# Kernel optimization log

Measured on AMD Instinct MI355X. Metric: run time of the kernel, lower is better.

Reference implementation:

```python
import jax, jax.numpy as jnp
import numpy as np

EPS_LN = 1e-5
NEG_SLOPE = 0.2
NUM_GRAPHS = 64


def layer_norm(h, g, b):
    mu = h.mean(-1, keepdims=True)
    var = ((h - mu) ** 2).mean(-1, keepdims=True)
    return (h - mu) * jax.lax.rsqrt(var + EPS_LN) * g + b


def segment_softmax(alpha, dst, n):
    # alpha: [E2, H], softmax over edges sharing the same dst node
    m = jax.ops.segment_max(alpha, dst, num_segments=n)
    m = jnp.where(jnp.isfinite(m), m, 0.0)
    e = jnp.exp(alpha - m[dst])
    s = jax.ops.segment_sum(e, dst, num_segments=n)
    return e / (s[dst] + 1e-16)


def gat_conv(h, src, dst, eattr, W, We, a_s, a_d, a_e, bias, H, C):
    # PyG GATConv: shared src/dst linear, edge features, self-loops (fill='mean')
    N = h.shape[0]
    x = (h @ W).reshape(N, H, C)  # [N,H,C]
    loop = jnp.arange(N)
    src2 = jnp.concatenate([src, loop])
    dst2 = jnp.concatenate([dst, loop])
    loop_attr = jnp.broadcast_to(eattr.mean(0, keepdims=True), (N, eattr.shape[1]))
    e2 = jnp.concatenate([eattr, loop_attr], 0)
    eh = (e2 @ We).reshape(-1, H, C)  # [E2,H,C]
    alpha = (x * a_s).sum(-1)[src2] + (x * a_d).sum(-1)[dst2] + (eh * a_e).sum(-1)
    alpha = jax.nn.leaky_relu(alpha, NEG_SLOPE)  # [E2,H]
    alpha = segment_softmax(alpha, dst2, N)
    out = jax.ops.segment_sum(x[src2] * alpha[:, :, None], dst2, num_segments=N)
    return out.reshape(N, H * C) + bias


def setup_inputs():
    key = jax.random.key(0)
    ks = jax.random.split(key, 24)
    N, E = 50000, 400000
    Fin, Hd, H, ed = 6, 64, 4, 1
    d0 = Hd * H          # 256 after layer0
    C1 = 128 // H        # 32, layer1 per-head out
    s = 0.1
    inp = {
        'x': jax.random.normal(ks[0], (N, Fin), jnp.float32),
        'edge_index': jax.random.randint(ks[1], (2, E), 0, N),
        'edge_attr': jax.random.uniform(ks[2], (E, ed), jnp.float32),
        'batch': jnp.sort(jax.random.randint(ks[3], (N,), 0, NUM_GRAPHS)),
        'W_in': jax.random.normal(ks[4], (Fin, Hd), jnp.float32) * s,
        'b_in': jnp.zeros((Hd,), jnp.float32),
        'l0_W': jax.random.normal(ks[5], (Hd, H * Hd), jnp.float32) * s,
        'l0_We': jax.random.normal(ks[6], (ed, H * Hd), jnp.float32) * s,
        'l0_as': jax.random.normal(ks[7], (H, Hd), jnp.float32) * s,
        'l0_ad': jax.random.normal(ks[8], (H, Hd), jnp.float32) * s,
        'l0_ae': jax.random.normal(ks[9], (H, Hd), jnp.float32) * s,
        'l0_b': jnp.zeros((H * Hd,), jnp.float32),
        'ln0_g': jnp.ones((d0,), jnp.float32),
        'ln0_b': jnp.zeros((d0,), jnp.float32),
        'l1_W': jax.random.normal(ks[10], (d0, H * C1), jnp.float32) * s,
        'l1_We': jax.random.normal(ks[11], (ed, H * C1), jnp.float32) * s,
        'l1_as': jax.random.normal(ks[12], (H, C1), jnp.float32) * s,
        'l1_ad': jax.random.normal(ks[13], (H, C1), jnp.float32) * s,
        'l1_ae': jax.random.normal(ks[14], (H, C1), jnp.float32) * s,
        'l1_b': jnp.zeros((H * C1,), jnp.float32),
        'ln1_g': jnp.ones((128,), jnp.float32),
        'ln1_b': jnp.zeros((128,), jnp.float32),
    }
    return inp


def reference(x, edge_index, edge_attr, batch, W_in, b_in,
              l0_W, l0_We, l0_as, l0_ad, l0_ae, l0_b, ln0_g, ln0_b,
              l1_W, l1_We, l1_as, l1_ad, l1_ae, l1_b, ln1_g, ln1_b):
    src, dst = edge_index[0], edge_index[1]
    H = 4
    h = x @ W_in + b_in                                  # input_proj
    h = gat_conv(h, src, dst, edge_attr, l0_W, l0_We, l0_as, l0_ad, l0_ae, l0_b, H, 64)
    h = layer_norm(h, ln0_g, ln0_b)
    h = jax.nn.elu(h)                                    # dropout off (eval)
    h = gat_conv(h, src, dst, edge_attr, l1_W, l1_We, l1_as, l1_ad, l1_ae, l1_b, H, 32)
    h = layer_norm(h, ln1_g, ln1_b)
    cnt = jax.ops.segment_sum(jnp.ones((h.shape[0],), h.dtype), batch, num_segments=NUM_GRAPHS)
    h_mean = jax.ops.segment_sum(h, batch, num_segments=NUM_GRAPHS) / jnp.maximum(cnt, 1.0)[:, None]
    h_max = jax.ops.segment_max(h, batch, num_segments=NUM_GRAPHS)
    return (h_mean + h_max) / 2.0
```

## Files before the change

### kernel.cpp

```cpp
#include <hip/hip_runtime.h>
#include <math.h>

#define EPS_LN   1e-5f
#define NEG_SLOPE 0.2f
#define NUM_GRAPHS 64
#define POOL_SPLIT 16

__device__ __forceinline__ float red64(float v) {
    #pragma unroll
    for (int m = 32; m > 0; m >>= 1) v += __shfl_xor(v, m);
    return v;
}

__global__ __launch_bounds__(256) void k_input_proj(
    const float* __restrict__ x, const float* __restrict__ Win,
    const float* __restrict__ bin, float* __restrict__ h, int N)
{
    int t = blockIdx.x * 256 + threadIdx.x;
    if (t >= N * 64) return;
    int n = t >> 6, c = t & 63;
    float acc = bin[c];
    const float* xr = x + n * 6;
    #pragma unroll
    for (int k = 0; k < 6; ++k) acc += xr[k] * Win[k * 64 + c];
    h[t] = acc;
}

__global__ __launch_bounds__(256) void k_prep(
    const float* __restrict__ We0, const float* __restrict__ ae0,
    const float* __restrict__ We1, const float* __restrict__ ae1,
    float* __restrict__ wedot0, float* __restrict__ wedot1)
{
    __shared__ float red[256];
    int t = threadIdx.x;
    red[t] = We0[t] * ae0[t];
    __syncthreads();
    for (int s = 32; s > 0; s >>= 1) { if ((t & 63) < s) red[t] += red[t + s]; __syncthreads(); }
    if ((t & 63) == 0) wedot0[t >> 6] = red[t];
    __syncthreads();
    red[t] = (t < 128) ? We1[t] * ae1[t] : 0.f;
    __syncthreads();
    for (int s = 16; s > 0; s >>= 1) { if (t < 128 && (t & 31) < s) red[t] += red[t + s]; __syncthreads(); }
    if (t < 128 && (t & 31) == 0) wedot1[t >> 5] = red[t];
}

__global__ __launch_bounds__(256) void k_esum_partial(const float* __restrict__ ea, float* __restrict__ part, int E)
{
    __shared__ float red[256];
    int t = threadIdx.x;
    float s = 0.f;
    for (int i = blockIdx.x * 256 + t; i < E; i += gridDim.x * 256) s += ea[i];
    red[t] = s; __syncthreads();
    for (int k = 128; k > 0; k >>= 1) { if (t < k) red[t] += red[t + k]; __syncthreads(); }
    if (t == 0) part[blockIdx.x] = red[0];
}
__global__ __launch_bounds__(256) void k_esum_final(const float* __restrict__ part, int B, float* __restrict__ mean_out, int E)
{
    __shared__ float red[256];
    int t = threadIdx.x;
    red[t] = (t < B) ? part[t] : 0.f; __syncthreads();
    for (int k = 128; k > 0; k >>= 1) { if (t < k) red[t] += red[t + k]; __syncthreads(); }
    if (t == 0) *mean_out = red[0] / (float)E;
}

__global__ __launch_bounds__(256) void k_counts_init(int* __restrict__ counts, int N)
{
    int t = blockIdx.x * 256 + threadIdx.x;
    if (t < N) counts[t] = 1;
}
__global__ __launch_bounds__(256) void k_count(const int* __restrict__ dst, int* __restrict__ counts, int E)
{
    int e = blockIdx.x * 256 + threadIdx.x;
    if (e < E) atomicAdd(&counts[dst[e]], 1);
}
__global__ __launch_bounds__(256) void k_scan_partial(const int* __restrict__ counts, int* __restrict__ bsum, int N)
{
    __shared__ int red[256];
    int b = blockIdx.x, t = threadIdx.x;
    int base = b * 1024 + t * 4;
    int s = 0;
    #pragma unroll
    for (int i = 0; i < 4; ++i) { int idx = base + i; if (idx < N) s += counts[idx]; }
    red[t] = s; __syncthreads();
    for (int k = 128; k > 0; k >>= 1) { if (t < k) red[t] += red[t + k]; __syncthreads(); }
    if (t == 0) bsum[b] = red[0];
}
__global__ __launch_bounds__(64) void k_scan_bsums(const int* __restrict__ bsum, int* __restrict__ bpre, int B)
{
    __shared__ int s[64];
    int t = threadIdx.x;
    int v = (t < B) ? bsum[t] : 0;
    s[t] = v; __syncthreads();
    for (int off = 1; off < 64; off <<= 1) {
        int u = (t >= off) ? s[t - off] : 0; __syncthreads();
        s[t] += u; __syncthreads();
    }
    if (t < B) bpre[t] = s[t] - v;
}
__global__ __launch_bounds__(256) void k_scan_chunk(
    const int* __restrict__ counts, const int* __restrict__ bpre,
    int* __restrict__ row_ptr, int* __restrict__ cursor, int N, int E2)
{
    __shared__ int s[256];
    int b = blockIdx.x, t = threadIdx.x;
    int base = b * 1024 + t * 4;
    int l0 = (base + 0 < N) ? counts[base + 0] : 0;
    int l1 = (base + 1 < N) ? counts[base + 1] : 0;
    int l2 = (base + 2 < N) ? counts[base + 2] : 0;
    int l3 = (base + 3 < N) ? counts[base + 3] : 0;
    int lsum = l0 + l1 + l2 + l3;
    s[t] = lsum; __syncthreads();
    for (int off = 1; off < 256; off <<= 1) {
        int u = (t >= off) ? s[t - off] : 0; __syncthreads();
        s[t] += u; __syncthreads();
    }
    int run = bpre[b] + s[t] - lsum;
    if (base + 0 < N) { row_ptr[base + 0] = run; cursor[base + 0] = run; } run += l0;
    if (base + 1 < N) { row_ptr[base + 1] = run; cursor[base + 1] = run; } run += l1;
    if (base + 2 < N) { row_ptr[base + 2] = run; cursor[base + 2] = run; } run += l2;
    if (base + 3 < N) { row_ptr[base + 3] = run; cursor[base + 3] = run; }
    if (b == 0 && t == 0) row_ptr[N] = E2;
}
__global__ __launch_bounds__(256) void k_place(
    const int* __restrict__ dst, int* __restrict__ cursor, int* __restrict__ eids, int E, int N)
{
    int e = blockIdx.x * 256 + threadIdx.x;
    if (e >= E + N) return;
    int d = (e < E) ? dst[e] : (e - E);
    int pos = atomicAdd(&cursor[d], 1);
    eids[pos] = e;
}
__global__ __launch_bounds__(256) void k_rowsort(const int* __restrict__ row_ptr, int* __restrict__ eids, int N)
{
    int n = blockIdx.x * 256 + threadIdx.x;
    if (n >= N) return;
    int r0 = row_ptr[n], r1 = row_ptr[n + 1];
    for (int i = r0 + 1; i < r1; ++i) {
        int key = eids[i];
        int j = i - 1;
        while (j >= r0 && eids[j] > key) { eids[j + 1] = eids[j]; --j; }
        eids[j + 1] = key;
    }
}

__global__ __launch_bounds__(256) void k_gemm0(
    const float* __restrict__ h, const float* __restrict__ W0,
    const float* __restrict__ As, const float* __restrict__ Ad,
    float* __restrict__ x0, float* __restrict__ as0, float* __restrict__ ad0, int N)
{
    __shared__ float Wc[32 * 128];
    __shared__ float Ht[32 * 128];
    const int nb = blockIdx.x * 128;
    const int q  = blockIdx.y;
    const int t = threadIdx.x;
    const int tc = t & 15, tr = t >> 4;
    const int r0 = tr * 4, c0 = tc * 4;
    const int kg = t & 7, rb = t >> 3;
    float asv[8], adv[8];
    #pragma unroll
    for (int j = 0; j < 8; ++j) {
        int col = q * 128 + c0 + ((j < 4) ? j : 60 + j);
        asv[j] = As[col]; adv[j] = Ad[col];
    }
    float acc[8][8] = {};
    #pragma unroll
    for (int kc = 0; kc < 2; ++kc) {
        __syncthreads();
        #pragma unroll
        for (int j = 0; j < 4; ++j) {
            int row = rb + j * 32;
            int n = nb + row;
            float4 v = make_float4(0.f, 0.f, 0.f, 0.f);
            if (n < N)
                v = *reinterpret_cast<const float4*>(h + (size_t)n * 64 + kc * 32 + kg * 4);
            #pragma unroll
            for (int i = 0; i < 4; ++i) {
                int k = kg * 4 + i;
                float e = (i == 0) ? v.x : (i == 1) ? v.y : (i == 2) ? v.z : v.w;
                Ht[k * 128 + (row ^ (k & 28))] = e;
            }
        }
        #pragma unroll
        for (int it = 0; it < 4; ++it) {
            int idx = t * 4 + it * 1024;
            int k2 = idx >> 7, c = idx & 127;
            *reinterpret_cast<float4*>(&Wc[idx]) =
                *reinterpret_cast<const float4*>(W0 + (size_t)(kc * 32 + k2) * 256 + q * 128 + c);
        }
        __syncthreads();
        #pragma unroll 4
        for (int k2 = 0; k2 < 32; ++k2) {
            int sw = k2 & 28;
            float4 hlo = *reinterpret_cast<const float4*>(&Ht[k2 * 128 + (r0 ^ sw)]);
            float4 hhi = *reinterpret_cast<const float4*>(&Ht[k2 * 128 + ((r0 + 64) ^ sw)]);
            float4 wlo = *reinterpret_cast<const float4*>(&Wc[k2 * 128 + c0]);
            float4 whi = *reinterpret_cast<const float4*>(&Wc[k2 * 128 + c0 + 64]);
            float hr[8] = {hlo.x, hlo.y, hlo.z, hlo.w, hhi.x, hhi.y, hhi.z, hhi.w};
            float wr[8] = {wlo.x, wlo.y, wlo.z, wlo.w, whi.x, whi.y, whi.z, whi.w};
            #pragma unroll
            for (int i = 0; i < 8; ++i)
                #pragma unroll
                for (int j = 0; j < 8; ++j)
                    acc[i][j] += hr[i] * wr[j];
        }
    }
    #pragma unroll
    for (int i = 0; i < 8; ++i) {
        int n = nb + ((i < 4) ? (r0 + i) : (r0 + 60 + i));
        if (n < N) {
            *reinterpret_cast<float4*>(x0 + (size_t)n * 256 + q * 128 + c0) =
                make_float4(acc[i][0], acc[i][1], acc[i][2], acc[i][3]);
            *reinterpret_cast<float4*>(x0 + (size_t)n * 256 + q * 128 + c0 + 64) =
                make_float4(acc[i][4], acc[i][5], acc[i][6], acc[i][7]);
        }
        float sA = acc[i][0] * asv[0] + acc[i][1] * asv[1] + acc[i][2] * asv[2] + acc[i][3] * asv[3];
        float sB = acc[i][4] * asv[4] + acc[i][5] * asv[5] + acc[i][6] * asv[6] + acc[i][7] * asv[7];
        float dA = acc[i][0] * adv[0] + acc[i][1] * adv[1] + acc[i][2] * adv[2] + acc[i][3] * adv[3];
        float dB = acc[i][4] * adv[4] + acc[i][5] * adv[5] + acc[i][6] * adv[6] + acc[i][7] * adv[7];
        #pragma unroll
        for (int off = 1; off <= 8; off <<= 1) {
            sA += __shfl_xor(sA, off); sB += __shfl_xor(sB, off);
            dA += __shfl_xor(dA, off); dB += __shfl_xor(dB, off);
        }
        if (tc == 0 && n < N) {
            as0[n * 4 + 2 * q] = sA; as0[n * 4 + 2 * q + 1] = sB;
            ad0[n * 4 + 2 * q] = dA; ad0[n * 4 + 2 * q + 1] = dB;
        }
    }
}

__global__ __launch_bounds__(256) void k_gemm1(
    const float* __restrict__ h0, const float* __restrict__ W1,
    const float* __restrict__ As, const float* __restrict__ Ad,
    float* __restrict__ x1, float* __restrict__ as1, float* __restrict__ ad1, int N)
{
    __shared__ float Wc[32 * 128];
    __shared__ float Ht[32 * 128];
    const int nb = blockIdx.x * 128;
    const int t = threadIdx.x;
    const int tc = t & 15, tr = t >> 4;
    const int r0 = tr * 4, c0 = tc * 4;
    const int kg = t & 7, rb = t >> 3;
    float asv[8], adv[8];
    #pragma unroll
    for (int j = 0; j < 8; ++j) {
        int col = c0 + ((j < 4) ? j : 60 + j);
        asv[j] = As[col]; adv[j] = Ad[col];
    }
    float acc[8][8] = {};
    for (int kc = 0; kc < 8; ++kc) {
        __syncthreads();
        #pragma unroll
        for (int j = 0; j < 4; ++j) {
            int row = rb + j * 32;
            int n = nb + row;
            float4 v = make_float4(0.f, 0.f, 0.f, 0.f);
            if (n < N)
                v = *reinterpret_cast<const float4*>(h0 + (size_t)n * 256 + kc * 32 + kg * 4);
            #pragma unroll
            for (int i = 0; i < 4; ++i) {
                int k = kg * 4 + i;
                float e = (i == 0) ? v.x : (i == 1) ? v.y : (i == 2) ? v.z : v.w;
                Ht[k * 128 + (row ^ (k & 28))] = e;
            }
        }
        #pragma unroll
        for (int it = 0; it < 4; ++it) {
            int idx = t * 4 + it * 1024;
            int k2 = idx >> 7, c = idx & 127;
            *reinterpret_cast<float4*>(&Wc[idx]) =
                *reinterpret_cast<const float4*>(W1 + (size_t)(kc * 32 + k2) * 128 + c);
        }
        __syncthreads();
        #pragma unroll 4
        for (int k2 = 0; k2 < 32; ++k2) {
            int sw = k2 & 28;
            float4 hlo = *reinterpret_cast<const float4*>(&Ht[k2 * 128 + (r0 ^ sw)]);
            float4 hhi = *reinterpret_cast<const float4*>(&Ht[k2 * 128 + ((r0 + 64) ^ sw)]);
            float4 wlo = *reinterpret_cast<const float4*>(&Wc[k2 * 128 + c0]);
            float4 whi = *reinterpret_cast<const float4*>(&Wc[k2 * 128 + c0 + 64]);
            float hr[8] = {hlo.x, hlo.y, hlo.z, hlo.w, hhi.x, hhi.y, hhi.z, hhi.w};
            float wr[8] = {wlo.x, wlo.y, wlo.z, wlo.w, whi.x, whi.y, whi.z, whi.w};
            #pragma unroll
            for (int i = 0; i < 8; ++i)
                #pragma unroll
                for (int j = 0; j < 8; ++j)
                    acc[i][j] += hr[i] * wr[j];
        }
    }
    #pragma unroll
    for (int i = 0; i < 8; ++i) {
        int n = nb + ((i < 4) ? (r0 + i) : (r0 + 60 + i));
        if (n < N) {
            *reinterpret_cast<float4*>(x1 + (size_t)n * 128 + c0) =
                make_float4(acc[i][0], acc[i][1], acc[i][2], acc[i][3]);
            *reinterpret_cast<float4*>(x1 + (size_t)n * 128 + c0 + 64) =
                make_float4(acc[i][4], acc[i][5], acc[i][6], acc[i][7]);
        }
        float sA = acc[i][0] * asv[0] + acc[i][1] * asv[1] + acc[i][2] * asv[2] + acc[i][3] * asv[3];
        float sB = acc[i][4] * asv[4] + acc[i][5] * asv[5] + acc[i][6] * asv[6] + acc[i][7] * asv[7];
        float dA = acc[i][0] * adv[0] + acc[i][1] * adv[1] + acc[i][2] * adv[2] + acc[i][3] * adv[3];
        float dB = acc[i][4] * adv[4] + acc[i][5] * adv[5] + acc[i][6] * adv[6] + acc[i][7] * adv[7];
        #pragma unroll
        for (int off = 1; off <= 4; off <<= 1) {
            sA += __shfl_xor(sA, off); sB += __shfl_xor(sB, off);
            dA += __shfl_xor(dA, off); dB += __shfl_xor(dB, off);
        }
        if ((tc & 7) == 0 && n < N) {
            int hA = tc >> 3;
            as1[n * 4 + hA] = sA; as1[n * 4 + 2 + hA] = sB;
            ad1[n * 4 + hA] = dA; ad1[n * 4 + 2 + hA] = dB;
        }
    }
}

template <bool WRITE_SRC>
__global__ __launch_bounds__(256) void k_edgeprep(
    const int* __restrict__ row_ptr, const int* __restrict__ eids,
    const int* __restrict__ src, const float* __restrict__ eattr,
    const float* __restrict__ emean_p, const float* __restrict__ wedot,
    const float* __restrict__ as_n, const float* __restrict__ ad_n,
    int* __restrict__ srcp, float4* __restrict__ alpha, float* __restrict__ sinv,
    int N, int E)
{
    int n = (blockIdx.x * 256 + threadIdx.x) >> 6;
    int lane = threadIdx.x & 63;
    if (n >= N) return;
    float emean = *emean_p;
    float wd0 = wedot[0], wd1 = wedot[1], wd2 = wedot[2], wd3 = wedot[3];
    float adv0 = ad_n[n * 4 + 0], adv1 = ad_n[n * 4 + 1];
    float adv2 = ad_n[n * 4 + 2], adv3 = ad_n[n * 4 + 3];
    int r0 = row_ptr[n], r1 = row_ptr[n + 1];

    float m0 = -1e30f, m1 = -1e30f, m2 = -1e30f, m3 = -1e30f;
    for (int i = r0 + lane; i < r1; i += 64) {
        int eid = eids[i];
        int sn; float ev;
        if (eid < E) { sn = src[eid]; ev = eattr[eid]; } else { sn = n; ev = emean; }
        if (WRITE_SRC) srcp[i] = sn;
        const float* as4 = as_n + (size_t)sn * 4;
        float a0 = as4[0] + adv0 + ev * wd0;
        float a1 = as4[1] + adv1 + ev * wd1;
        float a2 = as4[2] + adv2 + ev * wd2;
        float a3 = as4[3] + adv3 + ev * wd3;
        a0 = (a0 > 0.f) ? a0 : NEG_SLOPE * a0;
        a1 = (a1 > 0.f) ? a1 : NEG_SLOPE * a1;
        a2 = (a2 > 0.f) ? a2 : NEG_SLOPE * a2;
        a3 = (a3 > 0.f) ? a3 : NEG_SLOPE * a3;
        m0 = fmaxf(m0, a0); m1 = fmaxf(m1, a1);
        m2 = fmaxf(m2, a2); m3 = fmaxf(m3, a3);
        alpha[i] = make_float4(a0, a1, a2, a3);
    }
    #pragma unroll
    for (int off = 32; off > 0; off >>= 1) {
        m0 = fmaxf(m0, __shfl_xor(m0, off));
        m1 = fmaxf(m1, __shfl_xor(m1, off));
        m2 = fmaxf(m2, __shfl_xor(m2, off));
        m3 = fmaxf(m3, __shfl_xor(m3, off));
    }
    float s0 = 0.f, s1 = 0.f, s2 = 0.f, s3 = 0.f;
    for (int i = r0 + lane; i < r1; i += 64) {
        float4 a = alpha[i];
        float w0 = __expf(a.x - m0), w1 = __expf(a.y - m1);
        float w2 = __expf(a.z - m2), w3 = __expf(a.w - m3);
        s0 += w0; s1 += w1; s2 += w2; s3 += w3;
        alpha[i] = make_float4(w0, w1, w2, w3);
    }
    #pragma unroll
    for (int off = 32; off > 0; off >>= 1) {
        s0 += __shfl_xor(s0, off); s1 += __shfl_xor(s1, off);
        s2 += __shfl_xor(s2, off); s3 += __shfl_xor(s3, off);
    }
    if (lane == 0) {
        sinv[n * 4 + 0] = 1.f / (s0 + 1e-16f);
        sinv[n * 4 + 1] = 1.f / (s1 + 1e-16f);
        sinv[n * 4 + 2] = 1.f / (s2 + 1e-16f);
        sinv[n * 4 + 3] = 1.f / (s3 + 1e-16f);
    }
}

template <int HC, int VEC, bool DO_ELU>
__global__ __launch_bounds__(256) void k_agg(
    const float* __restrict__ x, const int* __restrict__ row_ptr,
    const int* __restrict__ srcp, const float* __restrict__ alpha,
    const float* __restrict__ sinv,
    const float* __restrict__ bias, const float* __restrict__ lng, const float* __restrict__ lnb,
    float* __restrict__ out, int N)
{
    int n = (blockIdx.x * 256 + threadIdx.x) >> 6;
    int lane = threadIdx.x & 63;
    if (n >= N) return;
    int hh = lane >> 4;
    int r0 = row_ptr[n], r1 = row_ptr[n + 1];

    float acc[VEC] = {};
    for (int i = r0; i < r1; i += 8) {
        int cnt = min(r1 - i, 8);
        int sn[8]; float wv[8];
        #pragma unroll
        for (int j = 0; j < 8; ++j)
            if (j < cnt) { sn[j] = srcp[i + j]; wv[j] = alpha[(size_t)(i + j) * 4 + hh]; }
        #pragma unroll
        for (int j = 0; j < 8; ++j)
            if (j < cnt) {
                const float* xr = x + (size_t)sn[j] * HC + lane * VEC;
                if constexpr (VEC == 4) {
                    float4 xv = *reinterpret_cast<const float4*>(xr);
                    acc[0] += wv[j] * xv.x; acc[1] += wv[j] * xv.y;
                    acc[2] += wv[j] * xv.z; acc[3] += wv[j] * xv.w;
                } else {
                    float2 xv = *reinterpret_cast<const float2*>(xr);
                    acc[0] += wv[j] * xv.x; acc[1] += wv[j] * xv.y;
                }
            }
    }
    float inv = sinv[n * 4 + hh];

    int ch0 = lane * VEC;
    float v[VEC];
    #pragma unroll
    for (int i = 0; i < VEC; ++i) v[i] = acc[i] * inv + bias[ch0 + i];
    float ls = 0.f;
    #pragma unroll
    for (int i = 0; i < VEC; ++i) ls += v[i];
    ls = red64(ls);
    float mu = ls / (float)HC;
    float lv = 0.f;
    #pragma unroll
    for (int i = 0; i < VEC; ++i) { float d = v[i] - mu; lv += d * d; }
    lv = red64(lv);
    float rs = rsqrtf(lv / (float)HC + EPS_LN);
    float o[VEC];
    #pragma unroll
    for (int i = 0; i < VEC; ++i) {
        float y = (v[i] - mu) * rs * lng[ch0 + i] + lnb[ch0 + i];
        if (DO_ELU) y = (y > 0.f) ? y : (expm1f(y));
        o[i] = y;
    }
    float* orow = out + (size_t)n * HC + ch0;
    if constexpr (VEC == 4) *reinterpret_cast<float4*>(orow) = make_float4(o[0], o[1], o[2], o[3]);
    else                    *reinterpret_cast<float2*>(orow) = make_float2(o[0], o[1]);
}

__global__ __launch_bounds__(128) void k_bounds(const int* __restrict__ batch, int* __restrict__ gstart, int N)
{
    int g = threadIdx.x;
    if (g > NUM_GRAPHS) return;
    int lo = 0, hi = N;
    while (lo < hi) { int mid = (lo + hi) >> 1; if (batch[mid] < g) lo = mid + 1; else hi = mid; }
    gstart[g] = lo;
}
__global__ __launch_bounds__(128) void k_pool1(
    const float* __restrict__ h1, const int* __restrict__ gstart,
    float* __restrict__ psum, float* __restrict__ pmax)
{
    int g = blockIdx.x, sl = blockIdx.y, c = threadIdx.x;
    int s0 = gstart[g], s1 = gstart[g + 1];
    int cnt = s1 - s0;
    int chunk = (cnt + POOL_SPLIT - 1) / POOL_SPLIT;
    int b0 = s0 + sl * chunk;
    int b1 = min(b0 + chunk, s1);
    float sum = 0.f, mx = -INFINITY;
    for (int n = b0; n < b1; ++n) {
        float v = h1[(size_t)n * 128 + c];
        sum += v; mx = fmaxf(mx, v);
    }
    int o = (g * POOL_SPLIT + sl) * 128 + c;
    psum[o] = sum; pmax[o] = mx;
}
__global__ __launch_bounds__(128) void k_pool2(
    const float* __restrict__ psum, const float* __restrict__ pmax,
    const int* __restrict__ gstart, float* __restrict__ out)
{
    int g = blockIdx.x, c = threadIdx.x;
    float sum = 0.f, mx = -INFINITY;
    #pragma unroll
    for (int sl = 0; sl < POOL_SPLIT; ++sl) {
        int o = (g * POOL_SPLIT + sl) * 128 + c;
        sum += psum[o];
        mx = fmaxf(mx, pmax[o]);
    }
    int cnt = gstart[g + 1] - gstart[g];
    float mean = sum / fmaxf((float)cnt, 1.f);
    out[g * 128 + c] = 0.5f * (mean + mx);
}

extern "C" void kernel_launch(void* const* d_in, const int* in_sizes, int n_in,
                              void* d_out, int out_size, void* d_ws, size_t ws_size,
                              hipStream_t stream)
{
    const float* x     = (const float*)d_in[0];
    const int*   ei    = (const int*)d_in[1];
    const float* eattr = (const float*)d_in[2];
    const int*   batch = (const int*)d_in[3];
    const float* Win   = (const float*)d_in[4];
    const float* bin   = (const float*)d_in[5];
    const float* l0W   = (const float*)d_in[6];
    const float* l0We  = (const float*)d_in[7];
    const float* l0as  = (const float*)d_in[8];
    const float* l0ad  = (const float*)d_in[9];
    const float* l0ae  = (const float*)d_in[10];
    const float* l0b   = (const float*)d_in[11];
    const float* ln0g  = (const float*)d_in[12];
    const float* ln0b  = (const float*)d_in[13];
    const float* l1W   = (const float*)d_in[14];
    const float* l1We  = (const float*)d_in[15];
    const float* l1as  = (const float*)d_in[16];
    const float* l1ad  = (const float*)d_in[17];
    const float* l1ae  = (const float*)d_in[18];
    const float* l1b   = (const float*)d_in[19];
    const float* ln1g  = (const float*)d_in[20];
    const float* ln1b  = (const float*)d_in[21];

    const int N = in_sizes[0] / 6;
    const int E = in_sizes[1] / 2;
    const int E2 = E + N;
    const int* srcI = ei;
    const int* dstI = ei + E;

    char* ws = (char*)d_ws;
    size_t off = 0;
    auto alloc = [&](size_t bytes) -> char* {
        char* p = ws + off;
        off += (bytes + 255) & ~(size_t)255;
        return p;
    };

    float* h      = (float*)alloc((size_t)N * 64 * 4);
    float* x0     = (float*)alloc((size_t)N * 256 * 4);
    float* h0     = (float*)alloc((size_t)N * 256 * 4);
    float* as0    = (float*)alloc((size_t)N * 4 * 4);
    float* ad0    = (float*)alloc((size_t)N * 4 * 4);
    float* as1    = (float*)alloc((size_t)N * 4 * 4);
    float* ad1    = (float*)alloc((size_t)N * 4 * 4);
    float* sinv   = (float*)alloc((size_t)N * 4 * 4);
    int*   row_ptr= (int*)alloc((size_t)(N + 1) * 4);
    int*   counts = (int*)alloc((size_t)N * 4);
    int*   cursor = (int*)alloc((size_t)N * 4);
    int*   eids   = (int*)alloc((size_t)E2 * 4);
    int*   srcp   = (int*)alloc((size_t)E2 * 4);
    float4* alphab= (float4*)alloc((size_t)E2 * 16);
    int*   bsum   = (int*)alloc(64 * 4);
    int*   bpre   = (int*)alloc(64 * 4);
    float* epart  = (float*)alloc(256 * 4);
    float* emean  = (float*)alloc(4);
    float* wedot0 = (float*)alloc(16);
    float* wedot1 = (float*)alloc(16);
    int*   gstart = (int*)alloc((NUM_GRAPHS + 1) * 4);
    float* psum   = (float*)alloc((size_t)NUM_GRAPHS * POOL_SPLIT * 128 * 4);
    float* pmax   = (float*)alloc((size_t)NUM_GRAPHS * POOL_SPLIT * 128 * 4);

    float* x1 = x0;
    float* h1 = x0 + (size_t)N * 128;

    const int B = (N + 1023) / 1024;

    k_input_proj<<<(N * 64 + 255) / 256, 256, 0, stream>>>(x, Win, bin, h, N);
    k_prep<<<1, 256, 0, stream>>>(l0We, l0ae, l1We, l1ae, wedot0, wedot1);
    k_esum_partial<<<256, 256, 0, stream>>>(eattr, epart, E);
    k_esum_final<<<1, 256, 0, stream>>>(epart, 256, emean, E);

    k_counts_init<<<(N + 255) / 256, 256, 0, stream>>>(counts, N);
    k_count<<<(E + 255) / 256, 256, 0, stream>>>(dstI, counts, E);
    k_scan_partial<<<B, 256, 0, stream>>>(counts, bsum, N);
    k_scan_bsums<<<1, 64, 0, stream>>>(bsum, bpre, B);
    k_scan_chunk<<<B, 256, 0, stream>>>(counts, bpre, row_ptr, cursor, N, E2);
    k_place<<<(E2 + 255) / 256, 256, 0, stream>>>(dstI, cursor, eids, E, N);
    k_rowsort<<<(N + 255) / 256, 256, 0, stream>>>(row_ptr, eids, N);

    k_gemm0<<<dim3((N + 127) / 128, 2), 256, 0, stream>>>(h, l0W, l0as, l0ad, x0, as0, ad0, N);
    k_edgeprep<true><<<(N + 3) / 4, 256, 0, stream>>>(
        row_ptr, eids, srcI, eattr, emean, wedot0, as0, ad0, srcp, alphab, sinv, N, E);
    k_agg<256, 4, true><<<(N + 3) / 4, 256, 0, stream>>>(
        x0, row_ptr, srcp, (const float*)alphab, sinv, l0b, ln0g, ln0b, h0, N);

    k_gemm1<<<(N + 127) / 128, 256, 0, stream>>>(h0, l1W, l1as, l1ad, x1, as1, ad1, N);
    k_edgeprep<false><<<(N + 3) / 4, 256, 0, stream>>>(
        row_ptr, eids, srcI, eattr, emean, wedot1, as1, ad1, srcp, alphab, sinv, N, E);
    k_agg<128, 2, false><<<(N + 3) / 4, 256, 0, stream>>>(
        x1, row_ptr, srcp, (const float*)alphab, sinv, l1b, ln1g, ln1b, h1, N);

    k_bounds<<<1, 128, 0, stream>>>(batch, gstart, N);
    k_pool1<<<dim3(NUM_GRAPHS, POOL_SPLIT), 128, 0, stream>>>(h1, gstart, psum, pmax);
    k_pool2<<<NUM_GRAPHS, 128, 0, stream>>>(psum, pmax, gstart, (float*)d_out);
}
```

Baseline: 391.7 us.

## Fuse input projection into gemm0 and edge softmax into aggregation via online softmax

Computes the 6-wide input projection inside k_gemm0's tile load instead of in a separate kernel that writes an intermediate h buffer. Removes k_edgeprep entirely: each aggregation wavefront now computes attention logits per edge and keeps an online (running max/rescale) softmax, so per-edge alpha and src buffers are no longer stored and reloaded. In exchange, the aggregation loop handles one edge at a time with a serial dependence, does two exps per edge per lane instead of sharing them, and loses the 8-way batching of gathers. The input projection is also recomputed in both gemm0 column blocks.

```diff
diff --git a/kernel.cpp b/kernel.cpp
--- a/kernel.cpp
+++ b/kernel.cpp
@@ -10,20 +10,6 @@
     #pragma unroll
     for (int m = 32; m > 0; m >>= 1) v += __shfl_xor(v, m);
     return v;
-}
-
-__global__ __launch_bounds__(256) void k_input_proj(
-    const float* __restrict__ x, const float* __restrict__ Win,
-    const float* __restrict__ bin, float* __restrict__ h, int N)
-{
-    int t = blockIdx.x * 256 + threadIdx.x;
-    if (t >= N * 64) return;
-    int n = t >> 6, c = t & 63;
-    float acc = bin[c];
-    const float* xr = x + n * 6;
-    #pragma unroll
-    for (int k = 0; k < 6; ++k) acc += xr[k] * Win[k * 64 + c];
-    h[t] = acc;
 }
 
 __global__ __launch_bounds__(256) void k_prep(
@@ -144,18 +130,24 @@
 }
 
 __global__ __launch_bounds__(256) void k_gemm0(
-    const float* __restrict__ h, const float* __restrict__ W0,
+    const float* __restrict__ x, const float* __restrict__ Win, const float* __restrict__ bin,
+    const float* __restrict__ W0,
     const float* __restrict__ As, const float* __restrict__ Ad,
     float* __restrict__ x0, float* __restrict__ as0, float* __restrict__ ad0, int N)
 {
     __shared__ float Wc[32 * 128];
     __shared__ float Ht[32 * 128];
+    __shared__ float Wi[6 * 64];
+    __shared__ float bi[64];
     const int nb = blockIdx.x * 128;
     const int q  = blockIdx.y;
     const int t = threadIdx.x;
     const int tc = t & 15, tr = t >> 4;
     const int r0 = tr * 4, c0 = tc * 4;
     const int kg = t & 7, rb = t >> 3;
+    if (t < 384 - 256) Wi[t + 256] = Win[t + 256];
+    Wi[t < 256 ? t : 0] = Win[t < 256 ? t : 0];
+    if (t < 64) bi[t] = bin[t];
     float asv[8], adv[8];
     #pragma unroll
     for (int j = 0; j < 8; ++j) {
@@ -170,14 +162,24 @@
         for (int j = 0; j < 4; ++j) {
             int row = rb + j * 32;
             int n = nb + row;
-            float4 v = make_float4(0.f, 0.f, 0.f, 0.f);
-            if (n < N)
-                v = *reinterpret_cast<const float4*>(h + (size_t)n * 64 + kc * 32 + kg * 4);
+            float hv[4] = {0.f, 0.f, 0.f, 0.f};
+            if (n < N) {
+                float xr[6];
+                #pragma unroll
+                for (int f = 0; f < 6; ++f) xr[f] = x[(size_t)n * 6 + f];
+                #pragma unroll
+                for (int i = 0; i < 4; ++i) {
+                    int k = kc * 32 + kg * 4 + i;
+                    float a = bi[k];
+                    #pragma unroll
+                    for (int f = 0; f < 6; ++f) a += xr[f] * Wi[f * 64 + k];
+                    hv[i] = a;
+                }
+            }
             #pragma unroll
             for (int i = 0; i < 4; ++i) {
                 int k = kg * 4 + i;
-                float e = (i == 0) ? v.x : (i == 1) ? v.y : (i == 2) ? v.z : v.w;
-                Ht[k * 128 + (row ^ (k & 28))] = e;
+                Ht[k * 128 + (row ^ (k & 28))] = hv[i];
             }
         }
         #pragma unroll
@@ -314,107 +316,52 @@
     }
 }
 
-template <bool WRITE_SRC>
-__global__ __launch_bounds__(256) void k_edgeprep(
-    const int* __restrict__ row_ptr, const int* __restrict__ eids,
-    const int* __restrict__ src, const float* __restrict__ eattr,
-    const float* __restrict__ emean_p, const float* __restrict__ wedot,
-    const float* __restrict__ as_n, const float* __restrict__ ad_n,
-    int* __restrict__ srcp, float4* __restrict__ alpha, float* __restrict__ sinv,
-    int N, int E)
-{
-    int n = (blockIdx.x * 256 + threadIdx.x) >> 6;
-    int lane = threadIdx.x & 63;
-    if (n >= N) return;
-    float emean = *emean_p;
-    float wd0 = wedot[0], wd1 = wedot[1], wd2 = wedot[2], wd3 = wedot[3];
-    float adv0 = ad_n[n * 4 + 0], adv1 = ad_n[n * 4 + 1];
-    float adv2 = ad_n[n * 4 + 2], adv3 = ad_n[n * 4 + 3];
-    int r0 = row_ptr[n], r1 = row_ptr[n + 1];
-
-    float m0 = -1e30f, m1 = -1e30f, m2 = -1e30f, m3 = -1e30f;
-    for (int i = r0 + lane; i < r1; i += 64) {
-        int eid = eids[i];
-        int sn; float ev;
-        if (eid < E) { sn = src[eid]; ev = eattr[eid]; } else { sn = n; ev = emean; }
-        if (WRITE_SRC) srcp[i] = sn;
-        const float* as4 = as_n + (size_t)sn * 4;
-        float a0 = as4[0] + adv0 + ev * wd0;
-        float a1 = as4[1] + adv1 + ev * wd1;
-        float a2 = as4[2] + adv2 + ev * wd2;
-        float a3 = as4[3] + adv3 + ev * wd3;
-        a0 = (a0 > 0.f) ? a0 : NEG_SLOPE * a0;
-        a1 = (a1 > 0.f) ? a1 : NEG_SLOPE * a1;
-        a2 = (a2 > 0.f) ? a2 : NEG_SLOPE * a2;
-        a3 = (a3 > 0.f) ? a3 : NEG_SLOPE * a3;
-        m0 = fmaxf(m0, a0); m1 = fmaxf(m1, a1);
-        m2 = fmaxf(m2, a2); m3 = fmaxf(m3, a3);
-        alpha[i] = make_float4(a0, a1, a2, a3);
-    }
-    #pragma unroll
-    for (int off = 32; off > 0; off >>= 1) {
-        m0 = fmaxf(m0, __shfl_xor(m0, off));
-        m1 = fmaxf(m1, __shfl_xor(m1, off));
-        m2 = fmaxf(m2, __shfl_xor(m2, off));
-        m3 = fmaxf(m3, __shfl_xor(m3, off));
-    }
-    float s0 = 0.f, s1 = 0.f, s2 = 0.f, s3 = 0.f;
-    for (int i = r0 + lane; i < r1; i += 64) {
-        float4 a = alpha[i];
-        float w0 = __expf(a.x - m0), w1 = __expf(a.y - m1);
-        float w2 = __expf(a.z - m2), w3 = __expf(a.w - m3);
-        s0 += w0; s1 += w1; s2 += w2; s3 += w3;
-        alpha[i] = make_float4(w0, w1, w2, w3);
-    }
-    #pragma unroll
-    for (int off = 32; off > 0; off >>= 1) {
-        s0 += __shfl_xor(s0, off); s1 += __shfl_xor(s1, off);
-        s2 += __shfl_xor(s2, off); s3 += __shfl_xor(s3, off);
-    }
-    if (lane == 0) {
-        sinv[n * 4 + 0] = 1.f / (s0 + 1e-16f);
-        sinv[n * 4 + 1] = 1.f / (s1 + 1e-16f);
-        sinv[n * 4 + 2] = 1.f / (s2 + 1e-16f);
-        sinv[n * 4 + 3] = 1.f / (s3 + 1e-16f);
-    }
-}
-
 template <int HC, int VEC, bool DO_ELU>
 __global__ __launch_bounds__(256) void k_agg(
-    const float* __restrict__ x, const int* __restrict__ row_ptr,
-    const int* __restrict__ srcp, const float* __restrict__ alpha,
-    const float* __restrict__ sinv,
+    const float* __restrict__ xbuf, const int* __restrict__ row_ptr,
+    const int* __restrict__ eids, const int* __restrict__ src,
+    const float* __restrict__ eattr, const float* __restrict__ emean_p,
+    const float* __restrict__ wedot,
+    const float* __restrict__ as_n, const float* __restrict__ ad_n,
     const float* __restrict__ bias, const float* __restrict__ lng, const float* __restrict__ lnb,
-    float* __restrict__ out, int N)
+    float* __restrict__ out, int N, int E)
 {
     int n = (blockIdx.x * 256 + threadIdx.x) >> 6;
     int lane = threadIdx.x & 63;
     if (n >= N) return;
     int hh = lane >> 4;
+    float wd = wedot[hh];
+    float adv = ad_n[n * 4 + hh];
+    float emean = *emean_p;
     int r0 = row_ptr[n], r1 = row_ptr[n + 1];
 
+    float m = -INFINITY, s = 0.f;
     float acc[VEC] = {};
-    for (int i = r0; i < r1; i += 8) {
-        int cnt = min(r1 - i, 8);
-        int sn[8]; float wv[8];
-        #pragma unroll
-        for (int j = 0; j < 8; ++j)
-            if (j < cnt) { sn[j] = srcp[i + j]; wv[j] = alpha[(size_t)(i + j) * 4 + hh]; }
-        #pragma unroll
-        for (int j = 0; j < 8; ++j)
-            if (j < cnt) {
-                const float* xr = x + (size_t)sn[j] * HC + lane * VEC;
-                if constexpr (VEC == 4) {
-                    float4 xv = *reinterpret_cast<const float4*>(xr);
-                    acc[0] += wv[j] * xv.x; acc[1] += wv[j] * xv.y;
-                    acc[2] += wv[j] * xv.z; acc[3] += wv[j] * xv.w;
-                } else {
-                    float2 xv = *reinterpret_cast<const float2*>(xr);
-                    acc[0] += wv[j] * xv.x; acc[1] += wv[j] * xv.y;
-                }
-            }
-    }
-    float inv = sinv[n * 4 + hh];
+    for (int i = r0; i < r1; ++i) {
+        int eid = eids[i];
+        int sn; float ev;
+        if (eid < E) { sn = src[eid]; ev = eattr[eid]; } else { sn = n; ev = emean; }
+        float a = as_n[(size_t)sn * 4 + hh] + adv + ev * wd;
+        a = (a > 0.f) ? a : NEG_SLOPE * a;
+        float nm = fmaxf(m, a);
+        float sc = __expf(m - nm);
+        float w  = __expf(a - nm);
+        m = nm;
+        s = s * sc + w;
+        const float* xr = xbuf + (size_t)sn * HC + lane * VEC;
+        if constexpr (VEC == 4) {
+            float4 xv = *reinterpret_cast<const float4*>(xr);
+            acc[0] = acc[0] * sc + w * xv.x;
+            acc[1] = acc[1] * sc + w * xv.y;
+            acc[2] = acc[2] * sc + w * xv.z;
+            acc[3] = acc[3] * sc + w * xv.w;
+        } else {
+            float2 xv = *reinterpret_cast<const float2*>(xr);
+            acc[0] = acc[0] * sc + w * xv.x;
+            acc[1] = acc[1] * sc + w * xv.y;
+        }
+    }
+    float inv = 1.f / (s + 1e-16f);
 
     int ch0 = lane * VEC;
     float v[VEC];
@@ -526,20 +473,16 @@
         return p;
     };
 
-    float* h      = (float*)alloc((size_t)N * 64 * 4);
     float* x0     = (float*)alloc((size_t)N * 256 * 4);
     float* h0     = (float*)alloc((size_t)N * 256 * 4);
     float* as0    = (float*)alloc((size_t)N * 4 * 4);
     float* ad0    = (float*)alloc((size_t)N * 4 * 4);
     float* as1    = (float*)alloc((size_t)N * 4 * 4);
     float* ad1    = (float*)alloc((size_t)N * 4 * 4);
-    float* sinv   = (float*)alloc((size_t)N * 4 * 4);
     int*   row_ptr= (int*)alloc((size_t)(N + 1) * 4);
     int*   counts = (int*)alloc((size_t)N * 4);
     int*   cursor = (int*)alloc((size_t)N * 4);
     int*   eids   = (int*)alloc((size_t)E2 * 4);
-    int*   srcp   = (int*)alloc((size_t)E2 * 4);
-    float4* alphab= (float4*)alloc((size_t)E2 * 16);
     int*   bsum   = (int*)alloc(64 * 4);
     int*   bpre   = (int*)alloc(64 * 4);
     float* epart  = (float*)alloc(256 * 4);
@@ -555,7 +498,6 @@
 
     const int B = (N + 1023) / 1024;
 
-    k_input_proj<<<(N * 64 + 255) / 256, 256, 0, stream>>>(x, Win, bin, h, N);
     k_prep<<<1, 256, 0, stream>>>(l0We, l0ae, l1We, l1ae, wedot0, wedot1);
     k_esum_partial<<<256, 256, 0, stream>>>(eattr, epart, E);
     k_esum_final<<<1, 256, 0, stream>>>(epart, 256, emean, E);
@@ -568,17 +510,16 @@
     k_place<<<(E2 + 255) / 256, 256, 0, stream>>>(dstI, cursor, eids, E, N);
     k_rowsort<<<(N + 255) / 256, 256, 0, stream>>>(row_ptr, eids, N);
 
-    k_gemm0<<<dim3((N + 127) / 128, 2), 256, 0, stream>>>(h, l0W, l0as, l0ad, x0, as0, ad0, N);
-    k_edgeprep<true><<<(N + 3) / 4, 256, 0, stream>>>(
-        row_ptr, eids, srcI, eattr, emean, wedot0, as0, ad0, srcp, alphab, sinv, N, E);
+    k_gemm0<<<dim3((N + 127) / 128, 2), 256, 0, stream>>>(
+        x, Win, bin, l0W, l0as, l0ad, x0, as0, ad0, N);
     k_agg<256, 4, true><<<(N + 3) / 4, 256, 0, stream>>>(
-        x0, row_ptr, srcp, (const float*)alphab, sinv, l0b, ln0g, ln0b, h0, N);
+        x0, row_ptr, eids, srcI, eattr, emean, wedot0, as0, ad0,
+        l0b, ln0g, ln0b, h0, N, E);
 
     k_gemm1<<<(N + 127) / 128, 256, 0, stream>>>(h0, l1W, l1as, l1ad, x1, as1, ad1, N);
-    k_edgeprep<false><<<(N + 3) / 4, 256, 0, stream>>>(
-        row_ptr, eids, srcI, eattr, emean, wedot1, as1, ad1, srcp, alphab, sinv, N, E);
     k_agg<128, 2, false><<<(N + 3) / 4, 256, 0, stream>>>(
-        x1, row_ptr, srcp, (const float*)alphab, sinv, l1b, ln1g, ln1b, h1, N);
+        x1, row_ptr, eids, srcI, eattr, emean, wedot1, as1, ad1,
+        l1b, ln1g, ln1b, h1, N, E);
 
     k_bounds<<<1, 128, 0, stream>>>(batch, gstart, N);
     k_pool1<<<dim3(NUM_GRAPHS, POOL_SPLIT), 128, 0, stream>>>(h1, gstart, psum, pmax);
```

Result: no change. 395.0 us (+0.8%).
